# Optimization experiments

Measured on AMD Instinct MI355X. Metric: run time of the kernel, lower is better.

Reference implementation:

```python
import jax, jax.numpy as jnp
import numpy as np


def _cdist_l2(a, b):
    # a: [b,k,D], b: [b,k,D] -> [b,k,k], matches torch.cdist(p=2)
    a2 = jnp.sum(a * a, axis=-1)[:, :, None]
    b2 = jnp.sum(b * b, axis=-1)[:, None, :]
    ab = jnp.einsum('bkd,bjd->bkj', a, b)
    return jnp.sqrt(jnp.maximum(a2 + b2 - 2.0 * ab, 0.0))


def _solve_lsa(cost):
    """Exact Hungarian (Jonker-Volgenant shortest augmenting path, O(n^3))
    on a square cost matrix [n,n]. Returns col_of_row: assigned column per row,
    identical to scipy.optimize.linear_sum_assignment's second return (first is arange).
    1-indexed arrays with a dummy slot 0, classic e-maxx formulation."""
    n = cost.shape[0]
    INF = jnp.float32(1e30)

    def row_body(i, carry):
        u, v, p = carry  # u,v: potentials [n+1]; p[j] = row matched to col j
        way = jnp.zeros(n + 1, jnp.int32)
        minv = jnp.full(n + 1, INF, jnp.float32)
        used = jnp.zeros(n + 1, bool)
        p = p.at[0].set(jnp.int32(i))

        def cond(c):
            j0, p, u, v, way, minv, used = c
            return p[j0] != 0

        def body(c):
            j0, p, u, v, way, minv, used = c
            used = used.at[j0].set(True)
            i0 = p[j0]
            cur = cost[i0 - 1, :] - u[i0] - v[1:]          # reduced costs, cols 1..n
            free = ~used[1:]
            better = free & (cur < minv[1:])
            minv = minv.at[1:].set(jnp.where(better, cur, minv[1:]))
            way = way.at[1:].set(jnp.where(better, j0, way[1:]))
            cand = jnp.where(free, minv[1:], INF)
            jmin = jnp.argmin(cand)
            delta = cand[jmin]
            j1 = (jmin + 1).astype(jnp.int32)
            u = u.at[p].add(jnp.where(used, delta, 0.0))   # u[p[j]] += delta for used j
            v = jnp.where(used, v - delta, v)
            minv = jnp.where(used, minv, minv - delta)
            return (j1, p, u, v, way, minv, used)

        j0 = jnp.int32(0)
        j0, p, u, v, way, minv, used = jax.lax.while_loop(
            cond, body, (j0, p, u, v, way, minv, used))

        # augment along alternating path
        def aug_cond(c):
            j0, p = c
            return j0 != 0

        def aug(c):
            j0, p = c
            j1 = way[j0]
            return (j1, p.at[j0].set(p[j1]))

        _, p = jax.lax.while_loop(aug_cond, aug, (j0, p))
        return (u, v, p)

    u0 = jnp.zeros(n + 1, jnp.float32)
    v0 = jnp.zeros(n + 1, jnp.float32)
    p0 = jnp.zeros(n + 1, jnp.int32)
    _, _, p = jax.lax.fori_loop(1, n + 1, row_body, (u0, v0, p0))
    # p[j] = row of col j  ->  invert to col of row
    col_of_row = jnp.zeros(n, jnp.int32).at[p[1:] - 1].set(jnp.arange(n, dtype=jnp.int32))
    return col_of_row


def setup_inputs() -> dict:
    key = jax.random.key(0)
    k1, k2 = jax.random.split(key)
    B, K, D = 16, 64, 50176  # b, k group masks, h*w = 224*224
    outputs = jax.random.normal(k1, (B, K, D), dtype=jnp.float32)
    targets = jax.random.normal(k2, (B, K, D), dtype=jnp.float32)
    return {"outputs": outputs, "targets": targets}


def reference(outputs, targets):
    # cost_type == 'L2'
    cost_mask = _cdist_l2(outputs, targets)                 # [b,k,k]
    inds2 = jax.vmap(_solve_lsa)(cost_mask)                 # [b,k] matched target idx per pred
    b, k = inds2.shape
    inds = jnp.broadcast_to(jnp.arange(k, dtype=jnp.int32), (b, k))  # scipy row_ind is arange
    return (inds, inds2)
```

## Files before the change

kernel.cpp:

```cpp
#include <hip/hip_runtime.h>

#define DD 50176
#define NB 16
#define NK 64
#define TK 64

template <int NSPLIT, int NTILE>
__global__ __launch_bounds__(256) void gemm_partial(const float* __restrict__ A,
                                                    const float* __restrict__ B,
                                                    float* __restrict__ ws) {
  const int s = blockIdx.x;
  const int b = blockIdx.y;
  const float* Ab = A + (size_t)b * NK * DD;
  const float* Bb = B + (size_t)b * NK * DD;
  __shared__ float As[TK * 64];
  __shared__ float Bs[TK * 64];
  const int tid = threadIdx.x;
  const int ti = tid & 15;
  const int tj = tid >> 4;
  const int kq = tid & 15;
  const int r0 = tid >> 4;

  float c[4][4] = {{0.f, 0.f, 0.f, 0.f}, {0.f, 0.f, 0.f, 0.f},
                   {0.f, 0.f, 0.f, 0.f}, {0.f, 0.f, 0.f, 0.f}};
  float a2p[4] = {0.f, 0.f, 0.f, 0.f};
  float b2p[4] = {0.f, 0.f, 0.f, 0.f};
  float4 avr[4], bvr[4];

  {
    const int k0 = s * NTILE * TK;
#pragma unroll
    for (int f = 0; f < 4; ++f) {
      const int r = f * 16 + r0;
      avr[f] = *reinterpret_cast<const float4*>(Ab + (size_t)r * DD + k0 + kq * 4);
      bvr[f] = *reinterpret_cast<const float4*>(Bb + (size_t)r * DD + k0 + kq * 4);
    }
  }

  for (int t = 0; t < NTILE; ++t) {
    __syncthreads();
#pragma unroll
    for (int f = 0; f < 4; ++f) {
      const int r = f * 16 + r0;
      const int col = (r + 4 * kq) & 63;
      const float4 av = avr[f];
      const float4 bv = bvr[f];
      As[(kq * 4 + 0) * 64 + col] = av.x;
      As[(kq * 4 + 1) * 64 + col] = av.y;
      As[(kq * 4 + 2) * 64 + col] = av.z;
      As[(kq * 4 + 3) * 64 + col] = av.w;
      Bs[(kq * 4 + 0) * 64 + col] = bv.x;
      Bs[(kq * 4 + 1) * 64 + col] = bv.y;
      Bs[(kq * 4 + 2) * 64 + col] = bv.z;
      Bs[(kq * 4 + 3) * 64 + col] = bv.w;
      a2p[f] = fmaf(av.x, av.x, a2p[f]); a2p[f] = fmaf(av.y, av.y, a2p[f]);
      a2p[f] = fmaf(av.z, av.z, a2p[f]); a2p[f] = fmaf(av.w, av.w, a2p[f]);
      b2p[f] = fmaf(bv.x, bv.x, b2p[f]); b2p[f] = fmaf(bv.y, bv.y, b2p[f]);
      b2p[f] = fmaf(bv.z, bv.z, b2p[f]); b2p[f] = fmaf(bv.w, bv.w, b2p[f]);
    }
    __syncthreads();

    if (t + 1 < NTILE) {
      const int k0 = (s * NTILE + t + 1) * TK;
#pragma unroll
      for (int f = 0; f < 4; ++f) {
        const int r = f * 16 + r0;
        avr[f] = *reinterpret_cast<const float4*>(Ab + (size_t)r * DD + k0 + kq * 4);
        bvr[f] = *reinterpret_cast<const float4*>(Bb + (size_t)r * DD + k0 + kq * 4);
      }
    }

#pragma unroll 8
    for (int kk = 0; kk < TK; ++kk) {
      const int g = 4 * (kk >> 2);
      const float4 a4 = *reinterpret_cast<const float4*>(&As[kk * 64 + ((4 * ti + g) & 63)]);
      const float4 b4 = *reinterpret_cast<const float4*>(&Bs[kk * 64 + ((4 * tj + g) & 63)]);
      const float ar[4] = {a4.x, a4.y, a4.z, a4.w};
      const float br[4] = {b4.x, b4.y, b4.z, b4.w};
#pragma unroll
      for (int r = 0; r < 4; ++r)
#pragma unroll
        for (int cc = 0; cc < 4; ++cc)
          c[r][cc] = fmaf(ar[r], br[cc], c[r][cc]);
    }
  }

  float* Pab = ws + (size_t)(b * NSPLIT + s) * 4096;
#pragma unroll
  for (int r = 0; r < 4; ++r) {
    *reinterpret_cast<float4*>(Pab + (ti * 4 + r) * 64 + tj * 4) =
        make_float4(c[r][0], c[r][1], c[r][2], c[r][3]);
  }

#pragma unroll
  for (int f = 0; f < 4; ++f) {
#pragma unroll
    for (int off = 1; off < 16; off <<= 1) {
      a2p[f] += __shfl_xor(a2p[f], off, 64);
      b2p[f] += __shfl_xor(b2p[f], off, 64);
    }
  }
  if (kq == 0) {
    float* Pa2 = ws + (size_t)NB * NSPLIT * 4096 + (size_t)(b * NSPLIT + s) * 64;
    float* Pb2 = Pa2 + (size_t)NB * NSPLIT * 64;
#pragma unroll
    for (int f = 0; f < 4; ++f) {
      Pa2[f * 16 + r0] = a2p[f];
      Pb2[f * 16 + r0] = b2p[f];
    }
  }
}

template <int NSPLIT>
__global__ __launch_bounds__(256) void reduce_cost(const float* __restrict__ ws,
                                                   float* __restrict__ costg) {
  const int slice = blockIdx.x;
  const int b = blockIdx.y;
  const int tid = threadIdx.x;
  __shared__ double a2s[4], b2s[64];
  const size_t pa2 = (size_t)NB * NSPLIT * 4096;
  const size_t pb2 = pa2 + (size_t)NB * NSPLIT * 64;

  if (tid < 64) {
    double s = 0.0;
    for (int sp = 0; sp < NSPLIT; ++sp)
      s += (double)ws[pb2 + (size_t)(b * NSPLIT + sp) * 64 + tid];
    b2s[tid] = s;
  } else if (tid < 68) {
    const int r = slice * 4 + (tid - 64);
    double s = 0.0;
    for (int sp = 0; sp < NSPLIT; ++sp)
      s += (double)ws[pa2 + (size_t)(b * NSPLIT + sp) * 64 + r];
    a2s[tid - 64] = s;
  }

  const int elem = slice * 256 + tid;
  double acc = 0.0;
  for (int sp = 0; sp < NSPLIT; ++sp)
    acc += (double)ws[(size_t)(b * NSPLIT + sp) * 4096 + elem];
  __syncthreads();

  const int ii = tid >> 6;
  const int j = tid & 63;
  const double c2 = a2s[ii] + b2s[j] - 2.0 * acc;
  costg[(size_t)b * 4096 + elem] = (float)sqrt(c2 > 0.0 ? c2 : 0.0);
}

__device__ __forceinline__ float readlane_f(float x, int lane) {
  return __int_as_float(__builtin_amdgcn_readlane(__float_as_int(x), lane));
}

template <int CTRL, int RMASK>
__device__ __forceinline__ float dpp_minf_step(float k) {
  const float o = __int_as_float(__builtin_amdgcn_update_dpp(
      0x7F800000 ,
      __float_as_int(k), CTRL, RMASK, 0xf, false));
  return fminf(o, k);
}
__device__ __forceinline__ float dpp_minf(float k) {
  k = dpp_minf_step<0x111, 0xf>(k);
  k = dpp_minf_step<0x112, 0xf>(k);
  k = dpp_minf_step<0x114, 0xf>(k);
  k = dpp_minf_step<0x118, 0xf>(k);
  k = dpp_minf_step<0x142, 0xa>(k);
  k = dpp_minf_step<0x143, 0xc>(k);
  return readlane_f(k, 63);
}

__global__ __launch_bounds__(64) void lsa_solve(const float* __restrict__ costg,
                                                int* __restrict__ out) {
  const int b = blockIdx.x;
  __shared__ float costd[64 * 64];
  const int tid = threadIdx.x;

  for (int e = tid; e < 4096; e += 64)
    costd[e] = costg[(size_t)b * 4096 + e];
  __syncthreads();

  const int l = tid;
  const float INFF = 1e30f;

  float cmin = costd[l];
  int cargmin = 0;
#pragma unroll 8
  for (int r = 1; r < 64; ++r) {
    const float cv = costd[r * 64 + l];
    if (cv < cmin) { cmin = cv; cargmin = r; }
  }
  float v_l = cmin;
  float u_l = 0.0f;
  int p_l = 0;
  int colof_l = 0;
  unsigned long long rowused = 0ULL;
  for (int j = 0; j < 64; ++j) {
    const int rj = __builtin_amdgcn_readlane(cargmin, j);
    if (!((rowused >> rj) & 1ULL)) {
      rowused |= 1ULL << rj;
      if (l == j) p_l = rj + 1;
      if (l == rj) colof_l = j + 1;
    }
  }
  unsigned long long freemask = ~rowused;

  {
    unsigned long long rm = rowused;
    while (rm) {
      const int ri = __ffsll(rm) - 1;
      rm &= rm - 1;
      const int j1 = __builtin_amdgcn_readlane(colof_l, ri) - 1;
      const float red = (l == j1) ? INFF : (costd[ri * 64 + l] - v_l);
      const float rmin = dpp_minf(red);
      if (l == ri) u_l = rmin;
      if (l == j1) v_l -= rmin;
    }
  }

  for (int pass = 0; pass < 2; ++pass) {
    unsigned long long m = freemask;
    while (m) {
      int ir = __ffsll(m);
      m &= m - 1;
      for (int chain = 0; chain < 8; ++chain) {
        if (!((freemask >> (ir - 1)) & 1ULL)) break;
        const float uir = readlane_f(u_l, ir - 1);
        const float curx = costd[(ir - 1) * 64 + l] - uir - v_l;
        const float u1 = dpp_minf(curx);
        const int j1 = __ffsll(__ballot(curx == u1)) - 1;
        const float cur2 = (l == j1) ? INFF : curx;
        const float u2 = dpp_minf(cur2);
        if (l == ir - 1) u_l = uir + u2;
        const bool strict = (u1 < u2);
        if (strict && l == j1) v_l -= (u2 - u1);
        const int k = __builtin_amdgcn_readlane(p_l, j1);
        if (strict || k == 0) {
          if (l == j1) p_l = ir;
          if (l == ir - 1) colof_l = j1 + 1;
          freemask &= ~(1ULL << (ir - 1));
          if (k != 0) {
            if (l == k - 1) colof_l = 0;
            freemask |= 1ULL << (k - 1);
            if (strict) { ir = k; continue; }
          }
          break;
        } else {
          break;
        }
      }
    }
  }

  for (int i_row = 1; i_row <= 64; ++i_row) {
    if (!((freemask >> (i_row - 1)) & 1ULL)) continue;
    float minv = INFF;
    int way_l = 0;
    bool used = false;
    int j0 = 0;
    const bool irow_hit = (l + 1 == i_row);

    while (true) {
      const int i0 = (j0 == 0) ? i_row : __builtin_amdgcn_readlane(p_l, j0 - 1);
      if (i0 == 0) break;
      if (j0 > 0 && l == j0 - 1) used = true;
      const unsigned long long um = __ballot(used);
      const bool addu = irow_hit ||
                        (colof_l != 0 && ((um >> (colof_l - 1)) & 1ULL));
      const float ui0 = readlane_f(u_l, i0 - 1);
      const float cur = costd[(i0 - 1) * 64 + l] - ui0 - v_l;
      if (!used && cur < minv) { minv = cur; way_l = j0; }
      const float cand = used ? INFF : minv;

      const float delta = dpp_minf(cand);
      const int jmin = __ffsll(__ballot(cand == delta)) - 1;

      if (used) v_l -= delta; else minv -= delta;
      if (addu) u_l += delta;
      j0 = jmin + 1;
    }

    while (j0 != 0) {
      const int j1 = __builtin_amdgcn_readlane(way_l, j0 - 1);
      const int pj1 = (j1 == 0) ? i_row : __builtin_amdgcn_readlane(p_l, j1 - 1);
      if (l == j0 - 1) p_l = pj1;
      if (l == pj1 - 1) colof_l = j0;
      j0 = j1;
    }
  }

  out[b * NK + l] = l;
  out[NB * NK + b * NK + l] = colof_l - 1;
}

extern "C" void kernel_launch(void* const* d_in, const int* in_sizes, int n_in,
                              void* d_out, int out_size, void* d_ws, size_t ws_size,
                              hipStream_t stream) {
  const float* A = (const float*)d_in[0];
  const float* B = (const float*)d_in[1];
  float* ws = (float*)d_ws;
  int* out = (int*)d_out;

  const size_t f112 = (size_t)NB * 112 * 4224;
  const size_t need112 = (f112 + (size_t)NB * 4096) * 4;

  if (ws_size >= need112) {
    float* costg = ws + f112;
    gemm_partial<112, 7><<<dim3(112, NB), 256, 0, stream>>>(A, B, ws);
    reduce_cost<112><<<dim3(16, NB), 256, 0, stream>>>(ws, costg);
    lsa_solve<<<NB, 64, 0, stream>>>(costg, out);
  } else {
    const size_t f49 = (size_t)NB * 49 * 4224;
    float* costg = ws + f49;
    gemm_partial<49, 16><<<dim3(49, NB), 256, 0, stream>>>(A, B, ws);
    reduce_cost<49><<<dim3(16, NB), 256, 0, stream>>>(ws, costg);
    lsa_solve<<<NB, 64, 0, stream>>>(costg, out);
  }
}
```

Measured before the change: 286.6 us.

## Give each wavefront its own K-split with an 8x8 register tile and no barriers

The GEMM partial kernel now gives each of the four wavefronts in a block its own K-slice, with private LDS tiles of 16 K-elements. Because staging is per-wavefront, the block-level __syncthreads calls are dropped. Each lane accumulates an 8x8 outer-product tile instead of 4x4, which raises FMA work per LDS load. The K split changes to 64 partials, and the workspace-size fallback path is removed. The cost is more registers per thread, which may lower occupancy. It also relies on wavefront-synchronous LDS access without explicit barriers, and assumes the workspace is large enough.

```diff
diff --git a/kernel.cpp b/kernel.cpp
--- a/kernel.cpp
+++ b/kernel.cpp
@@ -3,48 +3,53 @@
 #define DD 50176
 #define NB 16
 #define NK 64
-#define TK 64
-
-template <int NSPLIT, int NTILE>
+
+constexpr int KSPLIT = 64;
+constexpr int KTILE  = 49;
+constexpr int TKK    = 16;
+
 __global__ __launch_bounds__(256) void gemm_partial(const float* __restrict__ A,
                                                     const float* __restrict__ B,
                                                     float* __restrict__ ws) {
-  const int s = blockIdx.x;
   const int b = blockIdx.y;
+  const int w = threadIdx.x >> 6;
+  const int lane = threadIdx.x & 63;
+  const int s = blockIdx.x * 4 + w;
   const float* Ab = A + (size_t)b * NK * DD;
   const float* Bb = B + (size_t)b * NK * DD;
-  __shared__ float As[TK * 64];
-  __shared__ float Bs[TK * 64];
-  const int tid = threadIdx.x;
-  const int ti = tid & 15;
-  const int tj = tid >> 4;
-  const int kq = tid & 15;
-  const int r0 = tid >> 4;
-
-  float c[4][4] = {{0.f, 0.f, 0.f, 0.f}, {0.f, 0.f, 0.f, 0.f},
-                   {0.f, 0.f, 0.f, 0.f}, {0.f, 0.f, 0.f, 0.f}};
+
+  __shared__ __align__(16) float lds[4][2][TKK * 64];
+  float* As = lds[w][0];
+  float* Bs = lds[w][1];
+
+  const int ti = lane >> 3;
+  const int tj = lane & 7;
+  const int kq = lane & 3;
+  const int rr = lane >> 2;
+
+  float c[8][8];
+#pragma unroll
+  for (int r = 0; r < 8; ++r)
+#pragma unroll
+    for (int q = 0; q < 8; ++q) c[r][q] = 0.f;
   float a2p[4] = {0.f, 0.f, 0.f, 0.f};
   float b2p[4] = {0.f, 0.f, 0.f, 0.f};
   float4 avr[4], bvr[4];
 
-  {
-    const int k0 = s * NTILE * TK;
+  const int kbase = s * (KTILE * TKK);
+#pragma unroll
+  for (int f = 0; f < 4; ++f) {
+    const int row = f * 16 + rr;
+    avr[f] = *reinterpret_cast<const float4*>(Ab + (size_t)row * DD + kbase + kq * 4);
+    bvr[f] = *reinterpret_cast<const float4*>(Bb + (size_t)row * DD + kbase + kq * 4);
+  }
+
+  for (int t = 0; t < KTILE; ++t) {
 #pragma unroll
     for (int f = 0; f < 4; ++f) {
-      const int r = f * 16 + r0;
-      avr[f] = *reinterpret_cast<const float4*>(Ab + (size_t)r * DD + k0 + kq * 4);
-      bvr[f] = *reinterpret_cast<const float4*>(Bb + (size_t)r * DD + k0 + kq * 4);
-    }
-  }
-
-  for (int t = 0; t < NTILE; ++t) {
-    __syncthreads();
-#pragma unroll
-    for (int f = 0; f < 4; ++f) {
-      const int r = f * 16 + r0;
-      const int col = (r + 4 * kq) & 63;
-      const float4 av = avr[f];
-      const float4 bv = bvr[f];
+      const int row = f * 16 + rr;
+      const int col = (row + 8 * kq) & 63;
+      const float4 av = avr[f], bv = bvr[f];
       As[(kq * 4 + 0) * 64 + col] = av.x;
       As[(kq * 4 + 1) * 64 + col] = av.y;
       As[(kq * 4 + 2) * 64 + col] = av.z;
@@ -58,55 +63,55 @@
       b2p[f] = fmaf(bv.x, bv.x, b2p[f]); b2p[f] = fmaf(bv.y, bv.y, b2p[f]);
       b2p[f] = fmaf(bv.z, bv.z, b2p[f]); b2p[f] = fmaf(bv.w, bv.w, b2p[f]);
     }
-    __syncthreads();
-
-    if (t + 1 < NTILE) {
-      const int k0 = (s * NTILE + t + 1) * TK;
+    if (t + 1 < KTILE) {
+      const int k0 = kbase + (t + 1) * TKK;
 #pragma unroll
       for (int f = 0; f < 4; ++f) {
-        const int r = f * 16 + r0;
-        avr[f] = *reinterpret_cast<const float4*>(Ab + (size_t)r * DD + k0 + kq * 4);
-        bvr[f] = *reinterpret_cast<const float4*>(Bb + (size_t)r * DD + k0 + kq * 4);
+        const int row = f * 16 + rr;
+        avr[f] = *reinterpret_cast<const float4*>(Ab + (size_t)row * DD + k0 + kq * 4);
+        bvr[f] = *reinterpret_cast<const float4*>(Bb + (size_t)row * DD + k0 + kq * 4);
       }
     }
-
-#pragma unroll 8
-    for (int kk = 0; kk < TK; ++kk) {
-      const int g = 4 * (kk >> 2);
-      const float4 a4 = *reinterpret_cast<const float4*>(&As[kk * 64 + ((4 * ti + g) & 63)]);
-      const float4 b4 = *reinterpret_cast<const float4*>(&Bs[kk * 64 + ((4 * tj + g) & 63)]);
-      const float ar[4] = {a4.x, a4.y, a4.z, a4.w};
-      const float br[4] = {b4.x, b4.y, b4.z, b4.w};
-#pragma unroll
-      for (int r = 0; r < 4; ++r)
-#pragma unroll
-        for (int cc = 0; cc < 4; ++cc)
-          c[r][cc] = fmaf(ar[r], br[cc], c[r][cc]);
-    }
-  }
-
-  float* Pab = ws + (size_t)(b * NSPLIT + s) * 4096;
-#pragma unroll
-  for (int r = 0; r < 4; ++r) {
-    *reinterpret_cast<float4*>(Pab + (ti * 4 + r) * 64 + tj * 4) =
+#pragma unroll 4
+    for (int kk = 0; kk < TKK; ++kk) {
+      const int g = 8 * (kk >> 2);
+      const float4 a0 = *reinterpret_cast<const float4*>(&As[kk * 64 + ((8 * ti + g) & 63)]);
+      const float4 a1 = *reinterpret_cast<const float4*>(&As[kk * 64 + ((8 * ti + 4 + g) & 63)]);
+      const float4 b0 = *reinterpret_cast<const float4*>(&Bs[kk * 64 + ((8 * tj + g) & 63)]);
+      const float4 b1 = *reinterpret_cast<const float4*>(&Bs[kk * 64 + ((8 * tj + 4 + g) & 63)]);
+      const float ar[8] = {a0.x, a0.y, a0.z, a0.w, a1.x, a1.y, a1.z, a1.w};
+      const float br[8] = {b0.x, b0.y, b0.z, b0.w, b1.x, b1.y, b1.z, b1.w};
+#pragma unroll
+      for (int r = 0; r < 8; ++r)
+#pragma unroll
+        for (int q = 0; q < 8; ++q)
+          c[r][q] = fmaf(ar[r], br[q], c[r][q]);
+    }
+  }
+
+  float* Pab = ws + (size_t)(b * KSPLIT + s) * 4096;
+#pragma unroll
+  for (int r = 0; r < 8; ++r) {
+    *reinterpret_cast<float4*>(Pab + (8 * ti + r) * 64 + 8 * tj) =
         make_float4(c[r][0], c[r][1], c[r][2], c[r][3]);
+    *reinterpret_cast<float4*>(Pab + (8 * ti + r) * 64 + 8 * tj + 4) =
+        make_float4(c[r][4], c[r][5], c[r][6], c[r][7]);
   }
 
 #pragma unroll
   for (int f = 0; f < 4; ++f) {
-#pragma unroll
-    for (int off = 1; off < 16; off <<= 1) {
-      a2p[f] += __shfl_xor(a2p[f], off, 64);
-      b2p[f] += __shfl_xor(b2p[f], off, 64);
-    }
+    a2p[f] += __shfl_xor(a2p[f], 1, 64);
+    a2p[f] += __shfl_xor(a2p[f], 2, 64);
+    b2p[f] += __shfl_xor(b2p[f], 1, 64);
+    b2p[f] += __shfl_xor(b2p[f], 2, 64);
   }
   if (kq == 0) {
-    float* Pa2 = ws + (size_t)NB * NSPLIT * 4096 + (size_t)(b * NSPLIT + s) * 64;
-    float* Pb2 = Pa2 + (size_t)NB * NSPLIT * 64;
+    float* Pa2 = ws + (size_t)NB * KSPLIT * 4096 + (size_t)(b * KSPLIT + s) * 64;
+    float* Pb2 = Pa2 + (size_t)NB * KSPLIT * 64;
 #pragma unroll
     for (int f = 0; f < 4; ++f) {
-      Pa2[f * 16 + r0] = a2p[f];
-      Pb2[f * 16 + r0] = b2p[f];
+      Pa2[f * 16 + rr] = a2p[f];
+      Pb2[f * 16 + rr] = b2p[f];
     }
   }
 }
@@ -298,19 +303,10 @@
   float* ws = (float*)d_ws;
   int* out = (int*)d_out;
 
-  const size_t f112 = (size_t)NB * 112 * 4224;
-  const size_t need112 = (f112 + (size_t)NB * 4096) * 4;
-
-  if (ws_size >= need112) {
-    float* costg = ws + f112;
-    gemm_partial<112, 7><<<dim3(112, NB), 256, 0, stream>>>(A, B, ws);
-    reduce_cost<112><<<dim3(16, NB), 256, 0, stream>>>(ws, costg);
-    lsa_solve<<<NB, 64, 0, stream>>>(costg, out);
-  } else {
-    const size_t f49 = (size_t)NB * 49 * 4224;
-    float* costg = ws + f49;
-    gemm_partial<49, 16><<<dim3(49, NB), 256, 0, stream>>>(A, B, ws);
-    reduce_cost<49><<<dim3(16, NB), 256, 0, stream>>>(ws, costg);
-    lsa_solve<<<NB, 64, 0, stream>>>(costg, out);
-  }
-}
+  const size_t fpart = (size_t)NB * KSPLIT * 4224;
+  float* costg = ws + fpart;
+
+  gemm_partial<<<dim3(16, NB), 256, 0, stream>>>(A, B, ws);
+  reduce_cost<KSPLIT><<<dim3(16, NB), 256, 0, stream>>>(ws, costg);
+  lsa_solve<<<NB, 64, 0, stream>>>(costg, out);
+}
```

After: 264.6 us. 1.08x faster.
